# Performance work log

Hardware: AMD Instinct MI355X
Metric: run time of the kernel (lower is better)

The kernel has to match this reference:

```python
import jax, jax.numpy as jnp
import numpy as np

MP = 10242  # number of coarse (pooled) vertices = L.shape[0]


def setup_inputs() -> dict:
    key = jax.random.key(0)
    k1, k2, k3, k4 = jax.random.split(key, 4)
    B, M, F = 16, 40962, 128
    NNZ = 40968  # ~4 nonzeros per coarse vertex (barycentric pooling)
    x = jax.random.normal(k1, (B, M, F), dtype=jnp.float32)
    rows = jax.random.randint(k2, (NNZ,), 0, MP, dtype=jnp.int64)
    cols = jax.random.randint(k3, (NNZ,), 0, M, dtype=jnp.int64)
    vals = jax.random.uniform(k4, (NNZ,), dtype=jnp.float32)
    return {"x": x, "rows": rows, "cols": cols, "vals": vals}


def reference(x, rows, cols, vals):
    # Equivalent of tf.sparse_tensor_dense_matmul(L, reshape(transpose(x)))
    # L: sparse [Mp, M] in COO (rows, cols, vals); x: [B, M, F].
    # out[b, p, f] = sum_{k: rows[k]==p} vals[k] * x[b, cols[k], f]
    gathered = x[:, cols, :] * vals[None, :, None]          # [B, nnz, F]
    gathered = jnp.transpose(gathered, (1, 0, 2))           # [nnz, B, F]
    pooled = jax.ops.segment_sum(gathered, rows, num_segments=MP)  # [Mp, B, F]
    return jnp.transpose(pooled, (1, 0, 2))                 # [B, Mp, F]
```

## Files before the change

kernel.cpp:

```cpp
#include <hip/hip_runtime.h>

constexpr int MP  = 10242;
constexpr int B   = 16;
constexpr int M   = 40962;
constexpr int F   = 128;
constexpr int CAP = 32;

typedef float f32x4 __attribute__((ext_vector_type(4)));

__global__ void build_ell_kernel(const int* __restrict__ rows,
                                 const int* __restrict__ cols,
                                 const float* __restrict__ vals,
                                 int* __restrict__ counts,
                                 int2* __restrict__ ell,
                                 int nnz) {
    int k = blockIdx.x * blockDim.x + threadIdx.x;
    if (k < nnz) {
        int p = rows[k];
        int slot = atomicAdd(&counts[p], 1);
        if (slot < CAP) {
            ell[p * CAP + slot] = make_int2(cols[k], __float_as_int(vals[k]));
        }
    }
}

__global__ __launch_bounds__(256)
void pool_kernel(const float4* __restrict__ x,
                 const int* __restrict__ counts,
                 const int2* __restrict__ ell,
                 float4* __restrict__ out) {
    const int p    = blockIdx.x;
    const int q    = threadIdx.x >> 6;
    const int lane = threadIdx.x & 63;
    const int half = lane >> 5;
    const int l    = lane & 31;

    const int bA = (q << 1) | half;
    const int bB = bA + 8;

    int n = counts[p];
    n = n < CAP ? n : CAP;
    const int2* pe = ell + p * CAP;
    const float4* xA = x + (size_t)bA * (M * (F / 4));
    const float4* xB = x + (size_t)bB * (M * (F / 4));

    float4 accA; accA.x = accA.y = accA.z = accA.w = 0.f;
    float4 accB; accB.x = accB.y = accB.z = accB.w = 0.f;

    int j = 0;
    for (; j + 4 <= n; j += 4) {
        int2 e0 = pe[j], e1 = pe[j + 1], e2 = pe[j + 2], e3 = pe[j + 3];
        float4 a0 = xA[(size_t)e0.x * (F / 4) + l];
        float4 a1 = xA[(size_t)e1.x * (F / 4) + l];
        float4 a2 = xA[(size_t)e2.x * (F / 4) + l];
        float4 a3 = xA[(size_t)e3.x * (F / 4) + l];
        float4 c0 = xB[(size_t)e0.x * (F / 4) + l];
        float4 c1 = xB[(size_t)e1.x * (F / 4) + l];
        float4 c2 = xB[(size_t)e2.x * (F / 4) + l];
        float4 c3 = xB[(size_t)e3.x * (F / 4) + l];
        float v0 = __int_as_float(e0.y), v1 = __int_as_float(e1.y);
        float v2 = __int_as_float(e2.y), v3 = __int_as_float(e3.y);
        accA.x = fmaf(v0, a0.x, fmaf(v1, a1.x, fmaf(v2, a2.x, fmaf(v3, a3.x, accA.x))));
        accA.y = fmaf(v0, a0.y, fmaf(v1, a1.y, fmaf(v2, a2.y, fmaf(v3, a3.y, accA.y))));
        accA.z = fmaf(v0, a0.z, fmaf(v1, a1.z, fmaf(v2, a2.z, fmaf(v3, a3.z, accA.z))));
        accA.w = fmaf(v0, a0.w, fmaf(v1, a1.w, fmaf(v2, a2.w, fmaf(v3, a3.w, accA.w))));
        accB.x = fmaf(v0, c0.x, fmaf(v1, c1.x, fmaf(v2, c2.x, fmaf(v3, c3.x, accB.x))));
        accB.y = fmaf(v0, c0.y, fmaf(v1, c1.y, fmaf(v2, c2.y, fmaf(v3, c3.y, accB.y))));
        accB.z = fmaf(v0, c0.z, fmaf(v1, c1.z, fmaf(v2, c2.z, fmaf(v3, c3.z, accB.z))));
        accB.w = fmaf(v0, c0.w, fmaf(v1, c1.w, fmaf(v2, c2.w, fmaf(v3, c3.w, accB.w))));
    }
    for (; j < n; ++j) {
        int2 e = pe[j];
        float v = __int_as_float(e.y);
        float4 a = xA[(size_t)e.x * (F / 4) + l];
        float4 c = xB[(size_t)e.x * (F / 4) + l];
        accA.x = fmaf(v, a.x, accA.x);
        accA.y = fmaf(v, a.y, accA.y);
        accA.z = fmaf(v, a.z, accA.z);
        accA.w = fmaf(v, a.w, accA.w);
        accB.x = fmaf(v, c.x, accB.x);
        accB.y = fmaf(v, c.y, accB.y);
        accB.z = fmaf(v, c.z, accB.z);
        accB.w = fmaf(v, c.w, accB.w);
    }

    float4* oA = out + ((size_t)bA * MP + p) * (F / 4) + l;
    float4* oB = out + ((size_t)bB * MP + p) * (F / 4) + l;
    __builtin_nontemporal_store(*(const f32x4*)&accA, (f32x4*)oA);
    __builtin_nontemporal_store(*(const f32x4*)&accB, (f32x4*)oB);
}

extern "C" void kernel_launch(void* const* d_in, const int* in_sizes, int n_in,
                              void* d_out, int out_size, void* d_ws, size_t ws_size,
                              hipStream_t stream) {
    const float* x    = (const float*)d_in[0];
    const int*   rows = (const int*)d_in[1];
    const int*   cols = (const int*)d_in[2];
    const float* vals = (const float*)d_in[3];
    float* out = (float*)d_out;
    const int nnz = in_sizes[1];

    int*  counts = (int*)d_ws;
    int2* ell    = (int2*)(counts + MP);

    hipMemsetAsync(counts, 0, MP * sizeof(int), stream);

    int nb = (nnz + 255) / 256;
    build_ell_kernel<<<nb, 256, 0, stream>>>(rows, cols, vals, counts, ell, nnz);

    pool_kernel<<<MP, 256, 0, stream>>>((const float4*)x, counts, ell, (float4*)out);
}
```

Measured before the change: 462.2 us.

## Transpose referenced x rows into batch-contiguous layout before pooling gather

Marks which input vertices are referenced, then transposes only those rows of x into an [M, B*F] layout in workspace, so each pooling block reads one contiguous 8KB row per nonzero instead of 16 scattered 512B rows. The pooling kernel then gathers from the transposed buffer. This adds an extra pass that reads and writes roughly the used fraction of x (~63% of vertices with random cols), plus a larger workspace requirement. If the workspace is too small it falls back to the direct gather path.

```diff
diff --git a/kernel.cpp b/kernel.cpp
--- a/kernel.cpp
+++ b/kernel.cpp
@@ -13,30 +13,85 @@
                                  const float* __restrict__ vals,
                                  int* __restrict__ counts,
                                  int2* __restrict__ ell,
+                                 unsigned char* __restrict__ used,
                                  int nnz) {
     int k = blockIdx.x * blockDim.x + threadIdx.x;
     if (k < nnz) {
         int p = rows[k];
+        int c = cols[k];
+        if (used) used[c] = 1;
         int slot = atomicAdd(&counts[p], 1);
         if (slot < CAP) {
-            ell[p * CAP + slot] = make_int2(cols[k], __float_as_int(vals[k]));
+            ell[p * CAP + slot] = make_int2(c, __float_as_int(vals[k]));
         }
     }
 }
 
 __global__ __launch_bounds__(256)
-void pool_kernel(const float4* __restrict__ x,
-                 const int* __restrict__ counts,
-                 const int2* __restrict__ ell,
-                 float4* __restrict__ out) {
+void transpose_kernel(const float4* __restrict__ x,
+                      const unsigned char* __restrict__ used,
+                      float4* __restrict__ xt) {
+    int m = blockIdx.x * 4 + (threadIdx.x >> 6);
+    if (m >= M || !used[m]) return;
+    int lane = threadIdx.x & 63;
+    const float4* src = x + ((size_t)(lane >> 5) * M + (size_t)m) * 32 + (lane & 31);
+    float4*       dst = xt + (size_t)m * 512 + lane;
+    f32x4 v[8];
+#pragma unroll
+    for (int i = 0; i < 8; ++i)
+        v[i] = __builtin_nontemporal_load((const f32x4*)(src + (size_t)(2 * i) * M * 32));
+#pragma unroll
+    for (int i = 0; i < 8; ++i)
+        dst[i * 64] = *(float4*)&v[i];
+}
+
+__global__ __launch_bounds__(256)
+void pool_xt_kernel(const float4* __restrict__ xt,
+                    const int* __restrict__ counts,
+                    const int2* __restrict__ ell,
+                    float4* __restrict__ out) {
+    const int p = blockIdx.x;
+    const int t = threadIdx.x;
+    int n = counts[p];
+    n = n < CAP ? n : CAP;
+    const int2* pe = ell + p * CAP;
+
+    f32x4 acc0 = {0.f, 0.f, 0.f, 0.f}, acc1 = {0.f, 0.f, 0.f, 0.f};
+    int j = 0;
+    for (; j + 2 <= n; j += 2) {
+        int2 e0 = pe[j], e1 = pe[j + 1];
+        const f32x4* r0 = (const f32x4*)(xt + (size_t)e0.x * 512);
+        const f32x4* r1 = (const f32x4*)(xt + (size_t)e1.x * 512);
+        f32x4 a0 = r0[t], a1 = r0[t + 256];
+        f32x4 b0 = r1[t], b1 = r1[t + 256];
+        float v0 = __int_as_float(e0.y), v1 = __int_as_float(e1.y);
+        acc0 += v0 * a0; acc1 += v0 * a1;
+        acc0 += v1 * b0; acc1 += v1 * b1;
+    }
+    if (j < n) {
+        int2 e = pe[j];
+        const f32x4* r = (const f32x4*)(xt + (size_t)e.x * 512);
+        float v = __int_as_float(e.y);
+        acc0 += v * r[t]; acc1 += v * r[t + 256];
+    }
+    int b0i = t >> 5, l = t & 31;
+    f32x4* o0 = (f32x4*)(out + ((size_t)b0i * MP + p) * 32 + l);
+    f32x4* o1 = (f32x4*)(out + ((size_t)(b0i + 8) * MP + p) * 32 + l);
+    __builtin_nontemporal_store(acc0, o0);
+    __builtin_nontemporal_store(acc1, o1);
+}
+
+__global__ __launch_bounds__(256)
+void pool_direct_kernel(const float4* __restrict__ x,
+                        const int* __restrict__ counts,
+                        const int2* __restrict__ ell,
+                        float4* __restrict__ out) {
     const int p    = blockIdx.x;
     const int q    = threadIdx.x >> 6;
     const int lane = threadIdx.x & 63;
-    const int half = lane >> 5;
+    const int bA   = (q << 1) | (lane >> 5);
+    const int bB   = bA + 8;
     const int l    = lane & 31;
-
-    const int bA = (q << 1) | half;
-    const int bB = bA + 8;
 
     int n = counts[p];
     n = n < CAP ? n : CAP;
@@ -44,50 +99,19 @@
     const float4* xA = x + (size_t)bA * (M * (F / 4));
     const float4* xB = x + (size_t)bB * (M * (F / 4));
 
-    float4 accA; accA.x = accA.y = accA.z = accA.w = 0.f;
-    float4 accB; accB.x = accB.y = accB.z = accB.w = 0.f;
-
-    int j = 0;
-    for (; j + 4 <= n; j += 4) {
-        int2 e0 = pe[j], e1 = pe[j + 1], e2 = pe[j + 2], e3 = pe[j + 3];
-        float4 a0 = xA[(size_t)e0.x * (F / 4) + l];
-        float4 a1 = xA[(size_t)e1.x * (F / 4) + l];
-        float4 a2 = xA[(size_t)e2.x * (F / 4) + l];
-        float4 a3 = xA[(size_t)e3.x * (F / 4) + l];
-        float4 c0 = xB[(size_t)e0.x * (F / 4) + l];
-        float4 c1 = xB[(size_t)e1.x * (F / 4) + l];
-        float4 c2 = xB[(size_t)e2.x * (F / 4) + l];
-        float4 c3 = xB[(size_t)e3.x * (F / 4) + l];
-        float v0 = __int_as_float(e0.y), v1 = __int_as_float(e1.y);
-        float v2 = __int_as_float(e2.y), v3 = __int_as_float(e3.y);
-        accA.x = fmaf(v0, a0.x, fmaf(v1, a1.x, fmaf(v2, a2.x, fmaf(v3, a3.x, accA.x))));
-        accA.y = fmaf(v0, a0.y, fmaf(v1, a1.y, fmaf(v2, a2.y, fmaf(v3, a3.y, accA.y))));
-        accA.z = fmaf(v0, a0.z, fmaf(v1, a1.z, fmaf(v2, a2.z, fmaf(v3, a3.z, accA.z))));
-        accA.w = fmaf(v0, a0.w, fmaf(v1, a1.w, fmaf(v2, a2.w, fmaf(v3, a3.w, accA.w))));
-        accB.x = fmaf(v0, c0.x, fmaf(v1, c1.x, fmaf(v2, c2.x, fmaf(v3, c3.x, accB.x))));
-        accB.y = fmaf(v0, c0.y, fmaf(v1, c1.y, fmaf(v2, c2.y, fmaf(v3, c3.y, accB.y))));
-        accB.z = fmaf(v0, c0.z, fmaf(v1, c1.z, fmaf(v2, c2.z, fmaf(v3, c3.z, accB.z))));
-        accB.w = fmaf(v0, c0.w, fmaf(v1, c1.w, fmaf(v2, c2.w, fmaf(v3, c3.w, accB.w))));
-    }
-    for (; j < n; ++j) {
+    f32x4 accA = {0.f, 0.f, 0.f, 0.f}, accB = {0.f, 0.f, 0.f, 0.f};
+    for (int j = 0; j < n; ++j) {
         int2 e = pe[j];
         float v = __int_as_float(e.y);
-        float4 a = xA[(size_t)e.x * (F / 4) + l];
-        float4 c = xB[(size_t)e.x * (F / 4) + l];
-        accA.x = fmaf(v, a.x, accA.x);
-        accA.y = fmaf(v, a.y, accA.y);
-        accA.z = fmaf(v, a.z, accA.z);
-        accA.w = fmaf(v, a.w, accA.w);
-        accB.x = fmaf(v, c.x, accB.x);
-        accB.y = fmaf(v, c.y, accB.y);
-        accB.z = fmaf(v, c.z, accB.z);
-        accB.w = fmaf(v, c.w, accB.w);
+        f32x4 a = *(const f32x4*)&xA[(size_t)e.x * 32 + l];
+        f32x4 c = *(const f32x4*)&xB[(size_t)e.x * 32 + l];
+        accA += v * a;
+        accB += v * c;
     }
-
-    float4* oA = out + ((size_t)bA * MP + p) * (F / 4) + l;
-    float4* oB = out + ((size_t)bB * MP + p) * (F / 4) + l;
-    __builtin_nontemporal_store(*(const f32x4*)&accA, (f32x4*)oA);
-    __builtin_nontemporal_store(*(const f32x4*)&accB, (f32x4*)oB);
+    f32x4* oA = (f32x4*)(out + ((size_t)bA * MP + p) * 32 + l);
+    f32x4* oB = (f32x4*)(out + ((size_t)bB * MP + p) * 32 + l);
+    __builtin_nontemporal_store(accA, oA);
+    __builtin_nontemporal_store(accB, oB);
 }
 
 extern "C" void kernel_launch(void* const* d_in, const int* in_sizes, int n_in,
@@ -99,14 +123,36 @@
     const float* vals = (const float*)d_in[3];
     float* out = (float*)d_out;
     const int nnz = in_sizes[1];
+    const int nb  = (nnz + 255) / 256;
 
-    int*  counts = (int*)d_ws;
-    int2* ell    = (int2*)(counts + MP);
+    size_t xt_bytes   = (size_t)M * B * F * sizeof(float);
+    size_t counts_off = xt_bytes;
+    size_t ell_off    = counts_off + (size_t)MP * sizeof(int);
+    size_t used_off   = ell_off + (size_t)MP * CAP * sizeof(int2);
+    size_t needed     = used_off + (size_t)M;
 
-    hipMemsetAsync(counts, 0, MP * sizeof(int), stream);
+    if (ws_size >= needed) {
+        float* xt              = (float*)d_ws;
+        int*   counts          = (int*)((char*)d_ws + counts_off);
+        int2*  ell             = (int2*)((char*)d_ws + ell_off);
+        unsigned char* used    = (unsigned char*)((char*)d_ws + used_off);
 
-    int nb = (nnz + 255) / 256;
-    build_ell_kernel<<<nb, 256, 0, stream>>>(rows, cols, vals, counts, ell, nnz);
+        hipMemsetAsync(counts, 0, MP * sizeof(int), stream);
+        hipMemsetAsync(used, 0, M, stream);
 
-    pool_kernel<<<MP, 256, 0, stream>>>((const float4*)x, counts, ell, (float4*)out);
+        build_ell_kernel<<<nb, 256, 0, stream>>>(rows, cols, vals, counts, ell,
+                                                 used, nnz);
+        transpose_kernel<<<(M + 3) / 4, 256, 0, stream>>>((const float4*)x, used,
+                                                          (float4*)xt);
+        pool_xt_kernel<<<MP, 256, 0, stream>>>((const float4*)xt, counts, ell,
+                                               (float4*)out);
+    } else {
+        int*  counts = (int*)d_ws;
+        int2* ell    = (int2*)(counts + MP);
+        hipMemsetAsync(counts, 0, MP * sizeof(int), stream);
+        build_ell_kernel<<<nb, 256, 0, stream>>>(rows, cols, vals, counts, ell,
+                                                 (unsigned char*)nullptr, nnz);
+        pool_direct_kernel<<<MP, 256, 0, stream>>>((const float4*)x, counts, ell,
+                                                   (float4*)out);
+    }
 }
```

After: 524.7 us. 1.14x slower.
